# Optimization experiments

Measured on AMD Instinct MI355X. Metric: run time of the kernel, lower is better.

Reference implementation:

```python
import jax, jax.numpy as jnp
import numpy as np

ALPHA = 0.2    # LeakyReLU negative slope (init arg alpha)
HEADS = 8
EPS = 1e-5     # LayerNorm eps


def setup_inputs() -> dict:
    key = jax.random.key(0)
    ks = jax.random.split(key, 16)
    B, S, D = 4, 1024, 256
    dh = D // HEADS  # 32
    x = jax.random.normal(ks[0], (B, S, D), jnp.float32)
    adj = (jax.random.uniform(ks[1], (B, S, S)) < 0.05).astype(jnp.float32)
    adj = jnp.maximum(adj, jnp.eye(S, dtype=jnp.float32)[None])

    def w(k, shape, fan):
        return jax.random.normal(k, shape, jnp.float32) * (fan ** -0.5)

    # GAT layer 0: in->hidden (concat heads)
    W0 = w(ks[2], (D, D), D); a_src0 = w(ks[3], (HEADS, dh), dh); a_dst0 = w(ks[4], (HEADS, dh), dh)
    # GAT layer 1: hidden->hidden (concat heads)
    W1 = w(ks[5], (D, D), D); a_src1 = w(ks[6], (HEADS, dh), dh); a_dst1 = w(ks[7], (HEADS, dh), dh)
    # GAT layer 2: hidden->out (mean over heads, head_dim = out_dim)
    W2 = w(ks[8], (D, HEADS * D), D); a_src2 = w(ks[9], (HEADS, D), D); a_dst2 = w(ks[10], (HEADS, D), D)
    # LayerNorm
    ln_g = jnp.ones((D,), jnp.float32); ln_b = jnp.zeros((D,), jnp.float32)
    # FFN: D -> 2D -> D
    ff_w1 = w(ks[11], (D, 2 * D), D); ff_b1 = jnp.zeros((2 * D,), jnp.float32)
    ff_w2 = w(ks[12], (2 * D, D), 2 * D); ff_b2 = jnp.zeros((D,), jnp.float32)
    return dict(adj=adj, x=x, W0=W0, a_src0=a_src0, a_dst0=a_dst0,
                W1=W1, a_src1=a_src1, a_dst1=a_dst1,
                W2=W2, a_src2=a_src2, a_dst2=a_dst2,
                ln_g=ln_g, ln_b=ln_b,
                ff_w1=ff_w1, ff_b1=ff_b1, ff_w2=ff_w2, ff_b2=ff_b2)


def _gat_layer(h, adj, W, a_src, a_dst, concat):
    B, S, _ = h.shape
    hp = jnp.einsum('bsi,io->bso', h, W).reshape(B, S, HEADS, -1)  # [B,S,H,dh]
    src = jnp.einsum('bshd,hd->bsh', hp, a_src)  # per-node source score
    dst = jnp.einsum('bshd,hd->bsh', hp, a_dst)  # per-node dest score
    # e[b,i,j,h] = LeakyReLU(src_i + dst_j), masked by adjacency
    e = jax.nn.leaky_relu(src[:, :, None, :] + dst[:, None, :, :], ALPHA)
    e = jnp.where(adj[..., None] > 0, e, jnp.float32(-1e9))
    attn = jax.nn.softmax(e, axis=2)  # softmax over neighbors j
    out = jnp.einsum('bijh,bjhd->bihd', attn, hp)
    return out.reshape(B, S, -1) if concat else out.mean(axis=2)


def reference(adj, x, W0, a_src0, a_dst0, W1, a_src1, a_dst1, W2, a_src2, a_dst2,
              ln_g, ln_b, ff_w1, ff_b1, ff_w2, ff_b2):
    # MultiAttentionGAT: 3 layers with residuals, ELU between layers
    h = jax.nn.elu(_gat_layer(x, adj, W0, a_src0, a_dst0, True) + x)
    h = jax.nn.elu(_gat_layer(h, adj, W1, a_src1, a_dst1, True) + h)
    h = _gat_layer(h, adj, W2, a_src2, a_dst2, False) + h
    # LayerNorm
    mu = h.mean(-1, keepdims=True)
    var = h.var(-1, keepdims=True)
    h = (h - mu) * jax.lax.rsqrt(var + EPS) * ln_g + ln_b
    # GELU FFN + residual
    ff = jnp.dot(jax.nn.gelu(jnp.dot(h, ff_w1) + ff_b1), ff_w2) + ff_b2
    return h + ff
```

## Files before the change

kernel.cpp:

```cpp
#include <hip/hip_runtime.h>
#include <hip/hip_bf16.h>

#define B_ 4
#define S_ 1024
#define D_ 256
#define H_ 8
#define LRELU_ALPHA 0.2f
#define MAXDEG 128

typedef __attribute__((ext_vector_type(8))) short short8;
typedef __attribute__((ext_vector_type(4))) float floatx4;

__device__ __forceinline__ float bf2f(unsigned short u) {
    union { unsigned int i; float f; } c; c.i = ((unsigned int)u) << 16; return c.f;
}
__device__ __forceinline__ unsigned short f2bf(float f) {
    union { float f; unsigned int u; } c; c.f = f;
    unsigned int r = (c.u + 0x7FFF + ((c.u >> 16) & 1)) >> 16;
    return (unsigned short)r;
}

__device__ void castT_body(const float* __restrict__ W, unsigned short* __restrict__ out,
                           int K, int N, int k0, int n0, float (*t)[33], int tid) {
    int tx = tid & 31, ty = tid >> 5;
#pragma unroll
    for (int i = 0; i < 4; ++i)
        t[ty + 8 * i][tx] = W[(size_t)(k0 + ty + 8 * i) * N + n0 + tx];
    __syncthreads();
#pragma unroll
    for (int i = 0; i < 4; ++i)
        out[(size_t)(n0 + ty + 8 * i) * K + k0 + tx] = f2bf(t[tx][ty + 8 * i]);
}

__global__ __launch_bounds__(256) void k_prep(
        const float* __restrict__ x, unsigned short* __restrict__ xb,
        const float* __restrict__ W0, unsigned short* __restrict__ W0t,
        const float* __restrict__ W1, unsigned short* __restrict__ W1t,
        const float* __restrict__ W2, unsigned short* __restrict__ W2t,
        const float* __restrict__ F1, unsigned short* __restrict__ F1t,
        const float* __restrict__ F2, unsigned short* __restrict__ F2t,
        const float* __restrict__ as2, const float* __restrict__ ad2,
        float* __restrict__ WS2, float* __restrict__ WD2,
        const float* __restrict__ adj, int* __restrict__ nbr, int* __restrict__ cnt) {
    __shared__ float t[32][33];
    __shared__ int c;
    int b = blockIdx.x, tid = threadIdx.x;
    if (b < 1024) {
        int i = b * 256 + tid;
        float4 v = ((const float4*)x)[i];
        ushort4 u; u.x = f2bf(v.x); u.y = f2bf(v.y); u.z = f2bf(v.z); u.w = f2bf(v.w);
        ((ushort4*)xb)[i] = u;
    } else if (b < 1088) {
        int i = b - 1024; castT_body(W0, W0t, 256, 256, (i & 7) * 32, (i >> 3) * 32, t, tid);
    } else if (b < 1152) {
        int i = b - 1088; castT_body(W1, W1t, 256, 256, (i & 7) * 32, (i >> 3) * 32, t, tid);
    } else if (b < 1664) {
        int i = b - 1152;
        int k0 = (i & 7) * 32, d0 = ((i >> 3) & 7) * 32, h = i >> 6;
        int tx = tid & 31, ty = tid >> 5;
#pragma unroll
        for (int q = 0; q < 4; ++q)
            t[ty + 8 * q][tx] = W2[(size_t)(k0 + ty + 8 * q) * 2048 + h * 256 + d0 + tx];
        __syncthreads();
#pragma unroll
        for (int q = 0; q < 4; ++q)
            W2t[(size_t)(d0 + ty + 8 * q) * 2048 + h * 256 + k0 + tx] = f2bf(t[tx][ty + 8 * q]);
    } else if (b < 1792) {
        int i = b - 1664; castT_body(F1, F1t, 256, 512, (i & 7) * 32, (i >> 3) * 32, t, tid);
    } else if (b < 1920) {
        int i = b - 1792; castT_body(F2, F2t, 512, 256, (i & 15) * 32, (i >> 4) * 32, t, tid);
    } else if (b < 1928) {
        int h = b - 1920, k = tid;
        const float* wrow = W2 + (size_t)k * 2048 + h * 256;
        float s = 0.f, d = 0.f;
        for (int dd = 0; dd < 256; ++dd) {
            float w = wrow[dd];
            s += w * as2[h * 256 + dd];
            d += w * ad2[h * 256 + dd];
        }
        WS2[h * 256 + k] = s;
        WD2[h * 256 + k] = d;
    } else {
        int row = b - 1928;
        if (tid == 0) c = 0;
        __syncthreads();
        float4 a4 = ((const float4*)(adj + (size_t)row * S_))[tid];
#pragma unroll
        for (int q = 0; q < 4; ++q) {
            float a = q == 0 ? a4.x : q == 1 ? a4.y : q == 2 ? a4.z : a4.w;
            if (a > 0.f) {
                int s = atomicAdd(&c, 1);
                if (s < MAXDEG) nbr[row * MAXDEG + s] = tid * 4 + q;
            }
        }
        __syncthreads();
        if (tid == 0) cnt[row] = c < MAXDEG ? c : MAXDEG;
    }
}

__global__ __launch_bounds__(256) void k_gemm_wide(const unsigned short* __restrict__ A,
        const unsigned short* __restrict__ Bt, float* __restrict__ P,
        int M, int N, int K, int Kc) {
    __shared__ unsigned short As[64][40];
    __shared__ unsigned short Bs[256][40];
    int tid = threadIdx.x;
    int bm = blockIdx.y * 64, bn = blockIdx.x * 256;
    int kbeg = blockIdx.z * Kc, kend = kbeg + Kc;
    int lane = tid & 63, wv = tid >> 6;
    int lrow = lane & 15, lq = lane >> 4;
    floatx4 acc[4][4] = {};
    int sm = tid >> 2, skq = (tid & 3) * 8;
    const unsigned short* Ap = A + (size_t)(bm + sm) * K + skq;
    const unsigned short* Bp0 = Bt + (size_t)(bn + sm) * K + skq;
    const unsigned short* Bp1 = Bp0 + (size_t)64 * K;
    const unsigned short* Bp2 = Bp0 + (size_t)128 * K;
    const unsigned short* Bp3 = Bp0 + (size_t)192 * K;
    short8 av  = *(const short8*)(Ap + kbeg);
    short8 bv0 = *(const short8*)(Bp0 + kbeg);
    short8 bv1 = *(const short8*)(Bp1 + kbeg);
    short8 bv2 = *(const short8*)(Bp2 + kbeg);
    short8 bv3 = *(const short8*)(Bp3 + kbeg);
    for (int k0 = kbeg; k0 < kend; k0 += 32) {
        *(short8*)&As[sm][skq]        = av;
        *(short8*)&Bs[sm][skq]        = bv0;
        *(short8*)&Bs[sm + 64][skq]   = bv1;
        *(short8*)&Bs[sm + 128][skq]  = bv2;
        *(short8*)&Bs[sm + 192][skq]  = bv3;
        __syncthreads();
        if (k0 + 32 < kend) {
            av  = *(const short8*)(Ap + k0 + 32);
            bv0 = *(const short8*)(Bp0 + k0 + 32);
            bv1 = *(const short8*)(Bp1 + k0 + 32);
            bv2 = *(const short8*)(Bp2 + k0 + 32);
            bv3 = *(const short8*)(Bp3 + k0 + 32);
        }
        short8 aF[4], bF[4];
#pragma unroll
        for (int mi = 0; mi < 4; ++mi)
            aF[mi] = *(const short8*)&As[mi * 16 + lrow][lq * 8];
#pragma unroll
        for (int ni = 0; ni < 4; ++ni)
            bF[ni] = *(const short8*)&Bs[wv * 64 + ni * 16 + lrow][lq * 8];
#pragma unroll
        for (int mi = 0; mi < 4; ++mi)
#pragma unroll
            for (int ni = 0; ni < 4; ++ni)
                acc[mi][ni] = __builtin_amdgcn_mfma_f32_16x16x32_bf16(aF[mi], bF[ni], acc[mi][ni], 0, 0, 0);
        __syncthreads();
    }
    float* out = P + (size_t)blockIdx.z * M * N;
#pragma unroll
    for (int mi = 0; mi < 4; ++mi)
#pragma unroll
        for (int ni = 0; ni < 4; ++ni)
#pragma unroll
            for (int r = 0; r < 4; ++r) {
                int grow = bm + mi * 16 + lq * 4 + r;
                int gcol = bn + wv * 64 + ni * 16 + lrow;
                out[(size_t)grow * N + gcol] = acc[mi][ni][r];
            }
}

template<int EPI>
__global__ __launch_bounds__(256) void k_gemm64(
        const unsigned short* __restrict__ A, const unsigned short* __restrict__ Bt,
        int N, int K,
        float* __restrict__ Pout, unsigned short* __restrict__ Ob,
        const float* __restrict__ p1, const float* __restrict__ p2,
        float* __restrict__ SRC, float* __restrict__ DST) {
    __shared__ unsigned short As[64][40];
    __shared__ unsigned short Bs[64][40];
    int tid = threadIdx.x;
    int bm = blockIdx.y * 64, bn = blockIdx.x * 64;
    int lane = tid & 63, wv = tid >> 6;
    int lrow = lane & 15, lq = lane >> 4;
    floatx4 acc[4] = {};
    int sm = tid >> 2, skq = (tid & 3) * 8;
    const unsigned short* Ap = A + (size_t)(bm + sm) * K + skq;
    const unsigned short* Bp = Bt + (size_t)(bn + sm) * K + skq;
    short8 av = *(const short8*)Ap;
    short8 bv = *(const short8*)Bp;
    for (int k0 = 0; k0 < K; k0 += 32) {
        *(short8*)&As[sm][skq] = av;
        *(short8*)&Bs[sm][skq] = bv;
        __syncthreads();
        if (k0 + 32 < K) {
            av = *(const short8*)(Ap + k0 + 32);
            bv = *(const short8*)(Bp + k0 + 32);
        }
        short8 aF = *(const short8*)&As[wv * 16 + lrow][lq * 8];
        short8 bF[4];
#pragma unroll
        for (int ni = 0; ni < 4; ++ni)
            bF[ni] = *(const short8*)&Bs[ni * 16 + lrow][lq * 8];
#pragma unroll
        for (int ni = 0; ni < 4; ++ni)
            acc[ni] = __builtin_amdgcn_mfma_f32_16x16x32_bf16(aF, bF[ni], acc[ni], 0, 0, 0);
        __syncthreads();
    }
    int row0 = bm + wv * 16 + lq * 4;
    if (EPI == 0) {
#pragma unroll
        for (int ni = 0; ni < 4; ++ni)
#pragma unroll
            for (int r = 0; r < 4; ++r)
                Ob[(size_t)(row0 + r) * N + bn + ni * 16 + lrow] = f2bf(acc[ni][r]);
        float asv[4], adv[4];
#pragma unroll
        for (int ni = 0; ni < 4; ++ni) {
            asv[ni] = p1[bn + ni * 16 + lrow];
            adv[ni] = p2[bn + ni * 16 + lrow];
        }
#pragma unroll
        for (int r = 0; r < 4; ++r) {
            float sA = acc[0][r] * asv[0] + acc[1][r] * asv[1];
            float sB = acc[2][r] * asv[2] + acc[3][r] * asv[3];
            float dA = acc[0][r] * adv[0] + acc[1][r] * adv[1];
            float dB = acc[2][r] * adv[2] + acc[3][r] * adv[3];
#pragma unroll
            for (int o = 8; o; o >>= 1) {
                sA += __shfl_xor(sA, o); sB += __shfl_xor(sB, o);
                dA += __shfl_xor(dA, o); dB += __shfl_xor(dB, o);
            }
            if (lrow == 0) {
                int h0 = bn >> 5;
                SRC[(row0 + r) * 8 + h0]     = sA;
                SRC[(row0 + r) * 8 + h0 + 1] = sB;
                DST[(row0 + r) * 8 + h0]     = dA;
                DST[(row0 + r) * 8 + h0 + 1] = dB;
            }
        }
    } else if (EPI == 2) {
#pragma unroll
        for (int ni = 0; ni < 4; ++ni) {
            int gcol = bn + ni * 16 + lrow;
            float bb = p1[gcol];
#pragma unroll
            for (int r = 0; r < 4; ++r) {
                float xx = acc[ni][r] + bb;
                float tt = tanhf(0.7978845608028654f * (xx + 0.044715f * xx * xx * xx));
                Ob[(size_t)(row0 + r) * N + gcol] = f2bf(0.5f * xx * (1.f + tt));
            }
        }
    } else if (EPI == 3) {
#pragma unroll
        for (int ni = 0; ni < 4; ++ni) {
            int gcol = bn + ni * 16 + lrow;
            float bb = p1[gcol];
#pragma unroll
            for (int r = 0; r < 4; ++r) {
                float res = p2[(size_t)(row0 + r) * 256 + gcol];
                Pout[(size_t)(row0 + r) * 256 + gcol] = acc[ni][r] + bb + res;
            }
        }
    }
}

__global__ __launch_bounds__(256) void k_attn_small_f(const unsigned short* __restrict__ hp,
        const float* __restrict__ src, const float* __restrict__ dst,
        const int* __restrict__ nbr, const int* __restrict__ cnts,
        const float* __restrict__ X, float* __restrict__ Hout,
        unsigned short* __restrict__ Hb,
        const float* __restrict__ WS2, const float* __restrict__ WD2,
        float* __restrict__ SRC2, float* __restrict__ DST2) {
    int tid = threadIdx.x;
    int half = tid >> 7;
    int sub = tid & 127;
    int row = blockIdx.x * 2 + half;
    int rb = row & ~(S_ - 1);
    __shared__ int nb[2][MAXDEG];
    __shared__ float ss[2][8];
    __shared__ float ew[2][MAXDEG * 9];
    __shared__ float pr[2][2][16];
    int cnt = cnts[row];
    for (int t = sub; t < cnt; t += 128) nb[half][t] = nbr[row * MAXDEG + t];
    if (sub < 8) ss[half][sub] = src[row * H_ + sub];
    __syncthreads();
    for (int idx = sub; idx < cnt * 8; idx += 128) {
        int n = idx >> 3, h = idx & 7;
        int j = nb[half][n];
        float e = ss[half][h] + dst[(rb + j) * H_ + h];
        ew[half][n * 9 + h] = e > 0.f ? e : LRELU_ALPHA * e;
    }
    __syncthreads();
    {
        int wv2 = sub >> 6, lane = sub & 63;
        int h = wv2 * 4 + (lane >> 4), s16 = lane & 15;
        float m = -1e30f;
        for (int n = s16; n < cnt; n += 16) m = fmaxf(m, ew[half][n * 9 + h]);
        for (int o = 8; o; o >>= 1) m = fmaxf(m, __shfl_xor(m, o));
        float s = 0.f;
        for (int n = s16; n < cnt; n += 16) {
            float v = __expf(ew[half][n * 9 + h] - m); ew[half][n * 9 + h] = v; s += v;
        }
        for (int o = 8; o; o >>= 1) s += __shfl_xor(s, o);
        float inv = s > 0.f ? 1.f / s : 0.f;
        for (int n = s16; n < cnt; n += 16) ew[half][n * 9 + h] *= inv;
    }
    __syncthreads();
    int d0 = sub * 2;
    int h = sub >> 4;
    const unsigned short* hpb = hp + (size_t)rb * 256 + d0;
    const float* ewr = ew[half];
    float aA0 = 0.f, aA1 = 0.f, aB0 = 0.f, aB1 = 0.f;
    float aC0 = 0.f, aC1 = 0.f, aD0 = 0.f, aD1 = 0.f;
    int n = 0;
    for (; n + 3 < cnt; n += 4) {
        int j0 = nb[half][n], j1 = nb[half][n + 1];
        int j2 = nb[half][n + 2], j3 = nb[half][n + 3];
        unsigned int p0 = *(const unsigned int*)(hpb + (size_t)j0 * 256);
        unsigned int p1 = *(const unsigned int*)(hpb + (size_t)j1 * 256);
        unsigned int p2 = *(const unsigned int*)(hpb + (size_t)j2 * 256);
        unsigned int p3 = *(const unsigned int*)(hpb + (size_t)j3 * 256);
        float w0 = ewr[n * 9 + h], w1 = ewr[(n + 1) * 9 + h];
        float w2 = ewr[(n + 2) * 9 + h], w3 = ewr[(n + 3) * 9 + h];
        aA0 += w0 * bf2f((unsigned short)p0); aA1 += w0 * bf2f((unsigned short)(p0 >> 16));
        aB0 += w1 * bf2f((unsigned short)p1); aB1 += w1 * bf2f((unsigned short)(p1 >> 16));
        aC0 += w2 * bf2f((unsigned short)p2); aC1 += w2 * bf2f((unsigned short)(p2 >> 16));
        aD0 += w3 * bf2f((unsigned short)p3); aD1 += w3 * bf2f((unsigned short)(p3 >> 16));
    }
    for (; n < cnt; ++n) {
        int j = nb[half][n];
        unsigned int p = *(const unsigned int*)(hpb + (size_t)j * 256);
        float w = ewr[n * 9 + h];
        aA0 += w * bf2f((unsigned short)p); aA1 += w * bf2f((unsigned short)(p >> 16));
    }
    float2 xv = *(const float2*)(X + (size_t)row * 256 + d0);
    float ov0 = (aA0 + aB0) + (aC0 + aD0) + xv.x;
    float ov1 = (aA1 + aB1) + (aC1 + aD1) + xv.y;
    ov0 = ov0 > 0.f ? ov0 : (__expf(ov0) - 1.f);
    ov1 = ov1 > 0.f ? ov1 : (__expf(ov1) - 1.f);
    *(float2*)(Hout + (size_t)row * 256 + d0) = make_float2(ov0, ov1);
    ushort2 ub; ub.x = f2bf(ov0); ub.y = f2bf(ov1);
    *(ushort2*)(Hb + (size_t)row * 256 + d0) = ub;
    if (WS2 != nullptr) {
        int wv2 = sub >> 6, lane = sub & 63;
#pragma unroll
        for (int hh = 0; hh < 8; ++hh) {
            float sP = ov0 * WS2[hh * 256 + d0] + ov1 * WS2[hh * 256 + d0 + 1];
            float dP = ov0 * WD2[hh * 256 + d0] + ov1 * WD2[hh * 256 + d0 + 1];
            for (int o = 32; o; o >>= 1) { sP += __shfl_xor(sP, o); dP += __shfl_xor(dP, o); }
            if (lane == 0) { pr[half][wv2][hh * 2] = sP; pr[half][wv2][hh * 2 + 1] = dP; }
        }
        __syncthreads();
        if (sub < 16) {
            float tv = pr[half][0][sub] + pr[half][1][sub];
            if ((sub & 1) == 0) SRC2[row * 8 + (sub >> 1)] = tv;
            else                DST2[row * 8 + (sub >> 1)] = tv;
        }
    }
}

__global__ __launch_bounds__(256) void k_attn_Y(const unsigned short* __restrict__ Hb,
        const float* __restrict__ src2, const float* __restrict__ dst2,
        const int* __restrict__ nbr, const int* __restrict__ cnts,
        unsigned short* __restrict__ Ycat) {
    int row = blockIdx.x;
    int tid = threadIdx.x;
    int rb = row & ~(S_ - 1);
    __shared__ int nb[MAXDEG];
    __shared__ float ss[8];
    __shared__ float ew[MAXDEG * 8];
    int cnt = cnts[row];
    for (int t = tid; t < cnt; t += 256) nb[t] = nbr[row * MAXDEG + t];
    if (tid < 8) ss[tid] = src2[row * H_ + tid];
    __syncthreads();
    for (int idx = tid; idx < cnt * 8; idx += 256) {
        int n = idx >> 3, h = idx & 7;
        int j = nb[n];
        float e = ss[h] + dst2[(rb + j) * H_ + h];
        ew[n * 8 + h] = e > 0.f ? e : LRELU_ALPHA * e;
    }
    __syncthreads();
    {
        int lane = tid & 63, wv = tid >> 6;
        int h = wv * 2 + (lane >> 5), sub = lane & 31;
        float m = -1e30f;
        for (int n = sub; n < cnt; n += 32) m = fmaxf(m, ew[n * 8 + h]);
        for (int o = 16; o; o >>= 1) m = fmaxf(m, __shfl_xor(m, o));
        float s = 0.f;
        for (int n = sub; n < cnt; n += 32) {
            float v = __expf(ew[n * 8 + h] - m); ew[n * 8 + h] = v; s += v;
        }
        for (int o = 16; o; o >>= 1) s += __shfl_xor(s, o);
        float inv = s > 0.f ? 0.125f / s : 0.f;
        for (int n = sub; n < cnt; n += 32) ew[n * 8 + h] *= inv;
    }
    __syncthreads();
    int dp = tid & 127, hg = tid >> 7;
    const unsigned short* hbase = Hb + (size_t)rb * 256 + 2 * dp;
    const float* ewh = ew + hg * 4;
    float a0x = 0.f, a0y = 0.f, a0z = 0.f, a0w = 0.f;
    float a1x = 0.f, a1y = 0.f, a1z = 0.f, a1w = 0.f;
    int n = 0;
    for (; n + 3 < cnt; n += 4) {
        int j0 = nb[n], j1 = nb[n + 1], j2 = nb[n + 2], j3 = nb[n + 3];
        unsigned int p0 = *(const unsigned int*)(hbase + (size_t)j0 * 256);
        unsigned int p1 = *(const unsigned int*)(hbase + (size_t)j1 * 256);
        unsigned int p2 = *(const unsigned int*)(hbase + (size_t)j2 * 256);
        unsigned int p3 = *(const unsigned int*)(hbase + (size_t)j3 * 256);
        float4 w0 = *(const float4*)(ewh + n * 8);
        float4 w1 = *(const float4*)(ewh + (n + 1) * 8);
        float4 w2 = *(const float4*)(ewh + (n + 2) * 8);
        float4 w3 = *(const float4*)(ewh + (n + 3) * 8);
        float v0a = bf2f((unsigned short)p0), v0b = bf2f((unsigned short)(p0 >> 16));
        float v1a = bf2f((unsigned short)p1), v1b = bf2f((unsigned short)(p1 >> 16));
        float v2a = bf2f((unsigned short)p2), v2b = bf2f((unsigned short)(p2 >> 16));
        float v3a = bf2f((unsigned short)p3), v3b = bf2f((unsigned short)(p3 >> 16));
        a0x += w0.x * v0a + w1.x * v1a + w2.x * v2a + w3.x * v3a;
        a0y += w0.y * v0a + w1.y * v1a + w2.y * v2a + w3.y * v3a;
        a0z += w0.z * v0a + w1.z * v1a + w2.z * v2a + w3.z * v3a;
        a0w += w0.w * v0a + w1.w * v1a + w2.w * v2a + w3.w * v3a;
        a1x += w0.x * v0b + w1.x * v1b + w2.x * v2b + w3.x * v3b;
        a1y += w0.y * v0b + w1.y * v1b + w2.y * v2b + w3.y * v3b;
        a1z += w0.z * v0b + w1.z * v1b + w2.z * v2b + w3.z * v3b;
        a1w += w0.w * v0b + w1.w * v1b + w2.w * v2b + w3.w * v3b;
    }
    for (; n < cnt; ++n) {
        int j = nb[n];
        unsigned int p = *(const unsigned int*)(hbase + (size_t)j * 256);
        float4 w = *(const float4*)(ewh + n * 8);
        float va = bf2f((unsigned short)p), vb = bf2f((unsigned short)(p >> 16));
        a0x += w.x * va; a0y += w.y * va; a0z += w.z * va; a0w += w.w * va;
        a1x += w.x * vb; a1y += w.y * vb; a1z += w.z * vb; a1w += w.w * vb;
    }
    unsigned short* yb = Ycat + (size_t)row * 2048 + (hg * 4) * 256 + 2 * dp;
    ushort2 u;
    u.x = f2bf(a0x); u.y = f2bf(a1x); *(ushort2*)(yb)         = u;
    u.x = f2bf(a0y); u.y = f2bf(a1y); *(ushort2*)(yb + 256)   = u;
    u.x = f2bf(a0z); u.y = f2bf(a1z); *(ushort2*)(yb + 512)   = u;
    u.x = f2bf(a0w); u.y = f2bf(a1w); *(ushort2*)(yb + 768)   = u;
}

__global__ __launch_bounds__(256) void k_ln_red(const float* __restrict__ P, int nsplit,
        const float* __restrict__ Hres, const float* __restrict__ g,
        const float* __restrict__ bta, float* __restrict__ HLN,
        unsigned short* __restrict__ HLNb) {
    int row = blockIdx.x * 4 + (threadIdx.x >> 6);
    int lane = threadIdx.x & 63;
    float4 v = ((const float4*)(Hres + (size_t)row * 256))[lane];
    for (int sp = 0; sp < nsplit; ++sp) {
        float4 p = ((const float4*)(P + (size_t)sp * 1048576 + (size_t)row * 256))[lane];
        v.x += p.x; v.y += p.y; v.z += p.z; v.w += p.w;
    }
    float s = v.x + v.y + v.z + v.w;
    float q = v.x * v.x + v.y * v.y + v.z * v.z + v.w * v.w;
    for (int o = 32; o; o >>= 1) { s += __shfl_xor(s, o); q += __shfl_xor(q, o); }
    float mu = s * (1.f / 256.f);
    float var = q * (1.f / 256.f) - mu * mu;
    if (var < 0.f) var = 0.f;
    float rs = rsqrtf(var + 1e-5f);
    float4 gg = ((const float4*)g)[lane];
    float4 bb = ((const float4*)bta)[lane];
    float4 o;
    o.x = (v.x - mu) * rs * gg.x + bb.x;
    o.y = (v.y - mu) * rs * gg.y + bb.y;
    o.z = (v.z - mu) * rs * gg.z + bb.z;
    o.w = (v.w - mu) * rs * gg.w + bb.w;
    ((float4*)(HLN + (size_t)row * 256))[lane] = o;
    ushort4 ob; ob.x = f2bf(o.x); ob.y = f2bf(o.y); ob.z = f2bf(o.z); ob.w = f2bf(o.w);
    ((ushort4*)(HLNb + (size_t)row * 256))[lane] = ob;
}

extern "C" void kernel_launch(void* const* d_in, const int* in_sizes, int n_in,
                              void* d_out, int out_size, void* d_ws, size_t ws_size,
                              hipStream_t stream) {
    const float* adj   = (const float*)d_in[0];
    const float* x     = (const float*)d_in[1];
    const float* W0    = (const float*)d_in[2];
    const float* as0   = (const float*)d_in[3];
    const float* ad0   = (const float*)d_in[4];
    const float* W1    = (const float*)d_in[5];
    const float* as1   = (const float*)d_in[6];
    const float* ad1   = (const float*)d_in[7];
    const float* W2    = (const float*)d_in[8];
    const float* as2   = (const float*)d_in[9];
    const float* ad2   = (const float*)d_in[10];
    const float* ln_g  = (const float*)d_in[11];
    const float* ln_b  = (const float*)d_in[12];
    const float* ff_w1 = (const float*)d_in[13];
    const float* ff_b1 = (const float*)d_in[14];
    const float* ff_w2 = (const float*)d_in[15];
    const float* ff_b2 = (const float*)d_in[16];

    float* ws = (float*)d_ws;
    float* H    = ws;
    float* HLN  = ws + 1048576;
    unsigned short* Ycat = (unsigned short*)(ws + 2097152);
    unsigned short* HPb  = (unsigned short*)(ws + 6291456);
    unsigned short* xb   = (unsigned short*)(ws + 6815744);
    unsigned short* Hb   = (unsigned short*)(ws + 7340032);
    unsigned short* HLNb = (unsigned short*)(ws + 7864320);
    unsigned short* MIDb = (unsigned short*)(ws + 8388608);
    unsigned short* W0t  = (unsigned short*)(ws + 9437184);
    unsigned short* W1t  = (unsigned short*)(ws + 9469952);
    unsigned short* W2t  = (unsigned short*)(ws + 9502720);
    unsigned short* F1t  = (unsigned short*)(ws + 9764864);
    unsigned short* F2t  = (unsigned short*)(ws + 9830400);
    float* WS2  = ws + 9895936;
    float* WD2  = ws + 9897984;
    float* SRC  = ws + 9900032;
    float* DST  = ws + 9932800;
    float* SRC2 = ws + 9965568;
    float* DST2 = ws + 9998336;
    int*   NBR  = (int*)(ws + 10031104);
    int*   CNT  = (int*)(ws + 10555392);
    float* PP   = ws + 12582912;

    k_prep<<<6024, 256, 0, stream>>>(x, xb, W0, W0t, W1, W1t, W2, W2t,
                                     ff_w1, F1t, ff_w2, F2t, as2, ad2, WS2, WD2,
                                     adj, NBR, CNT);

    k_gemm64<0><<<dim3(4, 64), 256, 0, stream>>>(xb, W0t, 256, 256,
                                                 nullptr, HPb, as0, ad0, SRC, DST);
    k_attn_small_f<<<2048, 256, 0, stream>>>(HPb, SRC, DST, NBR, CNT, x, H, Hb,
                                             nullptr, nullptr, nullptr, nullptr);

    k_gemm64<0><<<dim3(4, 64), 256, 0, stream>>>(Hb, W1t, 256, 256,
                                                 nullptr, HPb, as1, ad1, SRC, DST);
    k_attn_small_f<<<2048, 256, 0, stream>>>(HPb, SRC, DST, NBR, CNT, H, H, Hb,
                                             WS2, WD2, SRC2, DST2);

    k_attn_Y<<<4096, 256, 0, stream>>>(Hb, SRC2, DST2, NBR, CNT, Ycat);
    k_gemm_wide<<<dim3(1, 64, 4), 256, 0, stream>>>(Ycat, W2t, PP, 4096, 256, 2048, 512);
    k_ln_red<<<1024, 256, 0, stream>>>(PP, 4, H, ln_g, ln_b, HLN, HLNb);

    k_gemm64<2><<<dim3(8, 64), 256, 0, stream>>>(HLNb, F1t, 512, 256,
                                                 nullptr, MIDb, ff_b1, nullptr, nullptr, nullptr);
    k_gemm64<3><<<dim3(4, 64), 256, 0, stream>>>(MIDb, F2t, 256, 512,
                                                 (float*)d_out, nullptr, ff_b2, HLN, nullptr, nullptr);
}
```

Measured before the change: 218.3 us.

## Fuse split-K reduction with LayerNorm via last-block atomic counter; double-buffer GEMM LDS

The wide layer-2 GEMM now splits K eight ways instead of four. The last block to finish each row tile, detected with an atomic counter, sums the partial products and applies the residual plus LayerNorm in place, so the separate k_ln_red kernel launch goes away. Both GEMM kernels now double-buffer their shared-memory tiles, which removes one barrier per K step. The W2 attention-weight projection in the prep kernel is rewritten as wave-parallel float4 loads with shuffle reductions, and the prep kernel also zeroes the counters. The cost is more partial-sum traffic, a serialized tail in the last block, and more LDS per block.

```diff
diff --git a/kernel.cpp b/kernel.cpp
--- a/kernel.cpp
+++ b/kernel.cpp
@@ -41,7 +41,8 @@
         const float* __restrict__ F2, unsigned short* __restrict__ F2t,
         const float* __restrict__ as2, const float* __restrict__ ad2,
         float* __restrict__ WS2, float* __restrict__ WD2,
-        const float* __restrict__ adj, int* __restrict__ nbr, int* __restrict__ cnt) {
+        const float* __restrict__ adj, int* __restrict__ nbr, int* __restrict__ cnt,
+        int* __restrict__ cnt2) {
     __shared__ float t[32][33];
     __shared__ int c;
     int b = blockIdx.x, tid = threadIdx.x;
@@ -69,19 +70,20 @@
         int i = b - 1664; castT_body(F1, F1t, 256, 512, (i & 7) * 32, (i >> 3) * 32, t, tid);
     } else if (b < 1920) {
         int i = b - 1792; castT_body(F2, F2t, 512, 256, (i & 15) * 32, (i >> 4) * 32, t, tid);
-    } else if (b < 1928) {
-        int h = b - 1920, k = tid;
-        const float* wrow = W2 + (size_t)k * 2048 + h * 256;
-        float s = 0.f, d = 0.f;
-        for (int dd = 0; dd < 256; ++dd) {
-            float w = wrow[dd];
-            s += w * as2[h * 256 + dd];
-            d += w * ad2[h * 256 + dd];
-        }
-        WS2[h * 256 + k] = s;
-        WD2[h * 256 + k] = d;
-    } else {
-        int row = b - 1928;
+    } else if (b < 2432) {
+        int id = (b - 1920) * 4 + (tid >> 6);
+        int h = id >> 8, k = id & 255;
+        int lane = tid & 63;
+        float4 w4 = *(const float4*)(W2 + (size_t)k * 2048 + h * 256 + lane * 4);
+        float4 a4 = *(const float4*)(as2 + h * 256 + lane * 4);
+        float4 d4 = *(const float4*)(ad2 + h * 256 + lane * 4);
+        float s = w4.x * a4.x + w4.y * a4.y + w4.z * a4.z + w4.w * a4.w;
+        float d = w4.x * d4.x + w4.y * d4.y + w4.z * d4.z + w4.w * d4.w;
+#pragma unroll
+        for (int o = 32; o; o >>= 1) { s += __shfl_xor(s, o); d += __shfl_xor(d, o); }
+        if (lane == 0) { WS2[h * 256 + k] = s; WD2[h * 256 + k] = d; }
+    } else if (b < 6528) {
+        int row = b - 2432;
         if (tid == 0) c = 0;
         __syncthreads();
         float4 a4 = ((const float4*)(adj + (size_t)row * S_))[tid];
@@ -95,23 +97,29 @@
         }
         __syncthreads();
         if (tid == 0) cnt[row] = c < MAXDEG ? c : MAXDEG;
-    }
-}
-
-__global__ __launch_bounds__(256) void k_gemm_wide(const unsigned short* __restrict__ A,
+    } else {
+        if (tid < 64) cnt2[tid] = 0;
+    }
+}
+
+__global__ __launch_bounds__(256) void k_gemm_wide_ln(const unsigned short* __restrict__ A,
         const unsigned short* __restrict__ Bt, float* __restrict__ P,
-        int M, int N, int K, int Kc) {
-    __shared__ unsigned short As[64][40];
-    __shared__ unsigned short Bs[256][40];
+        const float* __restrict__ Hres, const float* __restrict__ g,
+        const float* __restrict__ bta, float* __restrict__ HLN,
+        unsigned short* __restrict__ HLNb, int* __restrict__ cnt2) {
+    const int N = 256, K = 2048, Kc = 256;
+    __shared__ unsigned short As[2][64][40];
+    __shared__ unsigned short Bs[2][256][40];
+    __shared__ int lastflag;
     int tid = threadIdx.x;
-    int bm = blockIdx.y * 64, bn = blockIdx.x * 256;
+    int bm = blockIdx.y * 64;
     int kbeg = blockIdx.z * Kc, kend = kbeg + Kc;
     int lane = tid & 63, wv = tid >> 6;
     int lrow = lane & 15, lq = lane >> 4;
     floatx4 acc[4][4] = {};
     int sm = tid >> 2, skq = (tid & 3) * 8;
     const unsigned short* Ap = A + (size_t)(bm + sm) * K + skq;
-    const unsigned short* Bp0 = Bt + (size_t)(bn + sm) * K + skq;
+    const unsigned short* Bp0 = Bt + (size_t)sm * K + skq;
     const unsigned short* Bp1 = Bp0 + (size_t)64 * K;
     const unsigned short* Bp2 = Bp0 + (size_t)128 * K;
     const unsigned short* Bp3 = Bp0 + (size_t)192 * K;
@@ -120,14 +128,16 @@
     short8 bv1 = *(const short8*)(Bp1 + kbeg);
     short8 bv2 = *(const short8*)(Bp2 + kbeg);
     short8 bv3 = *(const short8*)(Bp3 + kbeg);
+    *(short8*)&As[0][sm][skq]       = av;
+    *(short8*)&Bs[0][sm][skq]       = bv0;
+    *(short8*)&Bs[0][sm + 64][skq]  = bv1;
+    *(short8*)&Bs[0][sm + 128][skq] = bv2;
+    *(short8*)&Bs[0][sm + 192][skq] = bv3;
+    __syncthreads();
+    int cur = 0;
     for (int k0 = kbeg; k0 < kend; k0 += 32) {
-        *(short8*)&As[sm][skq]        = av;
-        *(short8*)&Bs[sm][skq]        = bv0;
-        *(short8*)&Bs[sm + 64][skq]   = bv1;
-        *(short8*)&Bs[sm + 128][skq]  = bv2;
-        *(short8*)&Bs[sm + 192][skq]  = bv3;
-        __syncthreads();
-        if (k0 + 32 < kend) {
+        bool more = k0 + 32 < kend;
+        if (more) {
             av  = *(const short8*)(Ap + k0 + 32);
             bv0 = *(const short8*)(Bp0 + k0 + 32);
             bv1 = *(const short8*)(Bp1 + k0 + 32);
@@ -137,18 +147,26 @@
         short8 aF[4], bF[4];
 #pragma unroll
         for (int mi = 0; mi < 4; ++mi)
-            aF[mi] = *(const short8*)&As[mi * 16 + lrow][lq * 8];
+            aF[mi] = *(const short8*)&As[cur][mi * 16 + lrow][lq * 8];
 #pragma unroll
         for (int ni = 0; ni < 4; ++ni)
-            bF[ni] = *(const short8*)&Bs[wv * 64 + ni * 16 + lrow][lq * 8];
+            bF[ni] = *(const short8*)&Bs[cur][wv * 64 + ni * 16 + lrow][lq * 8];
 #pragma unroll
         for (int mi = 0; mi < 4; ++mi)
 #pragma unroll
             for (int ni = 0; ni < 4; ++ni)
                 acc[mi][ni] = __builtin_amdgcn_mfma_f32_16x16x32_bf16(aF[mi], bF[ni], acc[mi][ni], 0, 0, 0);
-        __syncthreads();
-    }
-    float* out = P + (size_t)blockIdx.z * M * N;
+        if (more) {
+            *(short8*)&As[cur ^ 1][sm][skq]       = av;
+            *(short8*)&Bs[cur ^ 1][sm][skq]       = bv0;
+            *(short8*)&Bs[cur ^ 1][sm + 64][skq]  = bv1;
+            *(short8*)&Bs[cur ^ 1][sm + 128][skq] = bv2;
+            *(short8*)&Bs[cur ^ 1][sm + 192][skq] = bv3;
+            __syncthreads();
+            cur ^= 1;
+        }
+    }
+    float* outP = P + (size_t)blockIdx.z * (1048576);
 #pragma unroll
     for (int mi = 0; mi < 4; ++mi)
 #pragma unroll
@@ -156,9 +174,43 @@
 #pragma unroll
             for (int r = 0; r < 4; ++r) {
                 int grow = bm + mi * 16 + lq * 4 + r;
-                int gcol = bn + wv * 64 + ni * 16 + lrow;
-                out[(size_t)grow * N + gcol] = acc[mi][ni][r];
+                int gcol = wv * 64 + ni * 16 + lrow;
+                outP[(size_t)grow * N + gcol] = acc[mi][ni][r];
             }
+    __threadfence();
+    __syncthreads();
+    if (tid == 0) lastflag = (atomicAdd(&cnt2[blockIdx.y], 1) == 7);
+    __syncthreads();
+    if (!lastflag) return;
+    __threadfence();
+    int rl = tid >> 6, ln2 = tid & 63;
+    for (int rr = 0; rr < 16; ++rr) {
+        int row = bm + rr * 4 + rl;
+        float4 v = ((const float4*)(Hres + (size_t)row * 256))[ln2];
+#pragma unroll
+        for (int sp = 0; sp < 8; ++sp) {
+            float4 p = ((const float4*)(P + (size_t)sp * 1048576 + (size_t)row * 256))[ln2];
+            v.x += p.x; v.y += p.y; v.z += p.z; v.w += p.w;
+        }
+        float s = v.x + v.y + v.z + v.w;
+        float q = v.x * v.x + v.y * v.y + v.z * v.z + v.w * v.w;
+#pragma unroll
+        for (int o = 32; o; o >>= 1) { s += __shfl_xor(s, o); q += __shfl_xor(q, o); }
+        float mu = s * (1.f / 256.f);
+        float var = q * (1.f / 256.f) - mu * mu;
+        if (var < 0.f) var = 0.f;
+        float rs = rsqrtf(var + 1e-5f);
+        float4 gg = ((const float4*)g)[ln2];
+        float4 bb = ((const float4*)bta)[ln2];
+        float4 o4;
+        o4.x = (v.x - mu) * rs * gg.x + bb.x;
+        o4.y = (v.y - mu) * rs * gg.y + bb.y;
+        o4.z = (v.z - mu) * rs * gg.z + bb.z;
+        o4.w = (v.w - mu) * rs * gg.w + bb.w;
+        ((float4*)(HLN + (size_t)row * 256))[ln2] = o4;
+        ushort4 ob; ob.x = f2bf(o4.x); ob.y = f2bf(o4.y); ob.z = f2bf(o4.z); ob.w = f2bf(o4.w);
+        ((ushort4*)(HLNb + (size_t)row * 256))[ln2] = ob;
+    }
 }
 
 template<int EPI>
@@ -168,8 +220,8 @@
         float* __restrict__ Pout, unsigned short* __restrict__ Ob,
         const float* __restrict__ p1, const float* __restrict__ p2,
         float* __restrict__ SRC, float* __restrict__ DST) {
-    __shared__ unsigned short As[64][40];
-    __shared__ unsigned short Bs[64][40];
+    __shared__ unsigned short As[2][64][40];
+    __shared__ unsigned short Bs[2][64][40];
     int tid = threadIdx.x;
     int bm = blockIdx.y * 64, bn = blockIdx.x * 64;
     int lane = tid & 63, wv = tid >> 6;
@@ -180,23 +232,30 @@
     const unsigned short* Bp = Bt + (size_t)(bn + sm) * K + skq;
     short8 av = *(const short8*)Ap;
     short8 bv = *(const short8*)Bp;
+    *(short8*)&As[0][sm][skq] = av;
+    *(short8*)&Bs[0][sm][skq] = bv;
+    __syncthreads();
+    int cur = 0;
     for (int k0 = 0; k0 < K; k0 += 32) {
-        *(short8*)&As[sm][skq] = av;
-        *(short8*)&Bs[sm][skq] = bv;
-        __syncthreads();
-        if (k0 + 32 < K) {
+        bool more = k0 + 32 < K;
+        if (more) {
             av = *(const short8*)(Ap + k0 + 32);
             bv = *(const short8*)(Bp + k0 + 32);
         }
-        short8 aF = *(const short8*)&As[wv * 16 + lrow][lq * 8];
+        short8 aF = *(const short8*)&As[cur][wv * 16 + lrow][lq * 8];
         short8 bF[4];
 #pragma unroll
         for (int ni = 0; ni < 4; ++ni)
-            bF[ni] = *(const short8*)&Bs[ni * 16 + lrow][lq * 8];
+            bF[ni] = *(const short8*)&Bs[cur][ni * 16 + lrow][lq * 8];
 #pragma unroll
         for (int ni = 0; ni < 4; ++ni)
             acc[ni] = __builtin_amdgcn_mfma_f32_16x16x32_bf16(aF, bF[ni], acc[ni], 0, 0, 0);
-        __syncthreads();
+        if (more) {
+            *(short8*)&As[cur ^ 1][sm][skq] = av;
+            *(short8*)&Bs[cur ^ 1][sm][skq] = bv;
+            __syncthreads();
+            cur ^= 1;
+        }
     }
     int row0 = bm + wv * 16 + lq * 4;
     if (EPI == 0) {
@@ -432,36 +491,6 @@
     u.x = f2bf(a0w); u.y = f2bf(a1w); *(ushort2*)(yb + 768)   = u;
 }
 
-__global__ __launch_bounds__(256) void k_ln_red(const float* __restrict__ P, int nsplit,
-        const float* __restrict__ Hres, const float* __restrict__ g,
-        const float* __restrict__ bta, float* __restrict__ HLN,
-        unsigned short* __restrict__ HLNb) {
-    int row = blockIdx.x * 4 + (threadIdx.x >> 6);
-    int lane = threadIdx.x & 63;
-    float4 v = ((const float4*)(Hres + (size_t)row * 256))[lane];
-    for (int sp = 0; sp < nsplit; ++sp) {
-        float4 p = ((const float4*)(P + (size_t)sp * 1048576 + (size_t)row * 256))[lane];
-        v.x += p.x; v.y += p.y; v.z += p.z; v.w += p.w;
-    }
-    float s = v.x + v.y + v.z + v.w;
-    float q = v.x * v.x + v.y * v.y + v.z * v.z + v.w * v.w;
-    for (int o = 32; o; o >>= 1) { s += __shfl_xor(s, o); q += __shfl_xor(q, o); }
-    float mu = s * (1.f / 256.f);
-    float var = q * (1.f / 256.f) - mu * mu;
-    if (var < 0.f) var = 0.f;
-    float rs = rsqrtf(var + 1e-5f);
-    float4 gg = ((const float4*)g)[lane];
-    float4 bb = ((const float4*)bta)[lane];
-    float4 o;
-    o.x = (v.x - mu) * rs * gg.x + bb.x;
-    o.y = (v.y - mu) * rs * gg.y + bb.y;
-    o.z = (v.z - mu) * rs * gg.z + bb.z;
-    o.w = (v.w - mu) * rs * gg.w + bb.w;
-    ((float4*)(HLN + (size_t)row * 256))[lane] = o;
-    ushort4 ob; ob.x = f2bf(o.x); ob.y = f2bf(o.y); ob.z = f2bf(o.z); ob.w = f2bf(o.w);
-    ((ushort4*)(HLNb + (size_t)row * 256))[lane] = ob;
-}
-
 extern "C" void kernel_launch(void* const* d_in, const int* in_sizes, int n_in,
                               void* d_out, int out_size, void* d_ws, size_t ws_size,
                               hipStream_t stream) {
@@ -505,11 +534,12 @@
     float* DST2 = ws + 9998336;
     int*   NBR  = (int*)(ws + 10031104);
     int*   CNT  = (int*)(ws + 10555392);
+    int*   CNT2 = (int*)(ws + 10559488);
     float* PP   = ws + 12582912;
 
-    k_prep<<<6024, 256, 0, stream>>>(x, xb, W0, W0t, W1, W1t, W2, W2t,
+    k_prep<<<6529, 256, 0, stream>>>(x, xb, W0, W0t, W1, W1t, W2, W2t,
                                      ff_w1, F1t, ff_w2, F2t, as2, ad2, WS2, WD2,
-                                     adj, NBR, CNT);
+                                     adj, NBR, CNT, CNT2);
 
     k_gemm64<0><<<dim3(4, 64), 256, 0, stream>>>(xb, W0t, 256, 256,
                                                  nullptr, HPb, as0, ad0, SRC, DST);
@@ -522,8 +552,8 @@
                                              WS2, WD2, SRC2, DST2);
 
     k_attn_Y<<<4096, 256, 0, stream>>>(Hb, SRC2, DST2, NBR, CNT, Ycat);
-    k_gemm_wide<<<dim3(1, 64, 4), 256, 0, stream>>>(Ycat, W2t, PP, 4096, 256, 2048, 512);
-    k_ln_red<<<1024, 256, 0, stream>>>(PP, 4, H, ln_g, ln_b, HLN, HLNb);
+    k_gemm_wide_ln<<<dim3(1, 64, 8), 256, 0, stream>>>(Ycat, W2t, PP, H, ln_g, ln_b,
+                                                       HLN, HLNb, CNT2);
 
     k_gemm64<2><<<dim3(8, 64), 256, 0, stream>>>(HLNb, F1t, 512, 256,
                                                  nullptr, MIDb, ff_b1, nullptr, nullptr, nullptr);
```

After: 297.5 us. 36.3% more time.
